# Kernel optimization log

Measured on AMD Instinct MI355X. Metric: run time of the kernel, lower is better.

Reference implementation:

```python
import jax, jax.numpy as jnp
import numpy as np

NOISE_DIM = 64
SEQ_DIM = 64
HIDDEN = 512
BATCH = 1024
N_STEPS = 512
INPUT_SIZE = SEQ_DIM + NOISE_DIM + 1  # 129


def setup_inputs() -> dict:
    key = jax.random.key(0)
    ks = jax.random.split(key, 8)
    s = 0.05
    return {
        "noise": jax.random.normal(ks[0], (BATCH, N_STEPS, NOISE_DIM), dtype=jnp.float32),
        "dts": jax.random.uniform(ks[1], (BATCH, N_STEPS, 1), dtype=jnp.float32),
        "W_ih": jax.random.normal(ks[2], (4 * HIDDEN, INPUT_SIZE), dtype=jnp.float32) * s,
        "W_hh": jax.random.normal(ks[3], (4 * HIDDEN, HIDDEN), dtype=jnp.float32) * s,
        "b_ih": jax.random.normal(ks[4], (4 * HIDDEN,), dtype=jnp.float32) * s,
        "b_hh": jax.random.normal(ks[5], (4 * HIDDEN,), dtype=jnp.float32) * s,
        "W_out": jax.random.normal(ks[6], (SEQ_DIM, HIDDEN), dtype=jnp.float32) * s,
        "b_out": jax.random.normal(ks[7], (SEQ_DIM,), dtype=jnp.float32) * s,
    }


def reference(noise, dts, W_ih, W_hh, b_ih, b_hh, W_out, b_out):
    B = noise.shape[0]
    H = W_hh.shape[1]
    last0 = jnp.zeros((B, SEQ_DIM), dtype=noise.dtype)
    h0 = jnp.zeros((B, H), dtype=noise.dtype)
    c0 = jnp.zeros((B, H), dtype=noise.dtype)
    b = b_ih + b_hh

    def step(carry, inp):
        last, h, c = carry
        n_t, dt_t = inp  # (B, noise_dim), (B, 1)
        x = jnp.concatenate([last, n_t, dt_t], axis=-1)  # (B, input_size)
        gates = x @ W_ih.T + h @ W_hh.T + b  # (B, 4H)
        i_g, f_g, g_g, o_g = jnp.split(gates, 4, axis=-1)
        c_new = jax.nn.sigmoid(f_g) * c + jax.nn.sigmoid(i_g) * jnp.tanh(g_g)
        h_new = jax.nn.sigmoid(o_g) * jnp.tanh(c_new)
        y = h_new @ W_out.T + b_out  # (B, seq_dim)
        return (y, h_new, c_new), y

    noise_t = jnp.swapaxes(noise, 0, 1)  # (n, B, noise_dim)
    dts_t = jnp.swapaxes(dts, 0, 1)  # (n, B, 1)
    (last, h, c), ys = jax.lax.scan(step, (last0, h0, c0), (noise_t, dts_t))
    gen_seq = jnp.swapaxes(ys, 0, 1)  # (B, n, seq_dim)
    return gen_seq, h[None, :, :], c[None, :, :]
```

## Files before the change

kernel.cpp:

```cpp
#include <hip/hip_runtime.h>
#include <stdint.h>


#define NGRP 32
#define KF_X 5
#define KF_H 32
#define KF_TOT 37
#define MAIN_FRAGS (8 * 8 * KF_TOT)
#define Y_FRAGS 64
#define TOT_FRAGS (MAIN_FRAGS + Y_FRAGS)
#define HOFF 33554432ull
#define COFF (HOFF + 524288ull)

typedef __attribute__((ext_vector_type(8))) short short8;
typedef __attribute__((ext_vector_type(4))) float f32x4;
typedef __attribute__((ext_vector_type(16))) float f32x16;
typedef __attribute__((ext_vector_type(4))) unsigned int u32x4;
typedef __attribute__((ext_vector_type(2))) unsigned int u32x2;

__device__ __forceinline__ unsigned short f2bf(float x) {
  unsigned int u = __float_as_uint(x);
  u += 0x7FFFu + ((u >> 16) & 1u);
  return (unsigned short)(u >> 16);
}
__device__ __forceinline__ unsigned int pk2(float a, float b) {
  return (unsigned)f2bf(a) | ((unsigned)f2bf(b) << 16);
}
__device__ __forceinline__ int uperm(int kz, int hi, int j) {
  return 64 * (kz >> 2) + 16 * (kz & 3) + 8 * (j >> 2) + 2 * (j & 3) + hi;
}

__global__ void prep_pack(const float* __restrict__ Wih,
                          const float* __restrict__ Whh,
                          const float* __restrict__ bih,
                          const float* __restrict__ bhh,
                          const float* __restrict__ Wout,
                          const float* __restrict__ bout,
                          unsigned short* __restrict__ pack,
                          int* __restrict__ flags) {
  int tid = blockIdx.x * blockDim.x + threadIdx.x;
  if (blockIdx.x == 0) {
    for (int i = threadIdx.x; i < NGRP * 256; i += blockDim.x) flags[i] = 0;
  }
  int fi = tid >> 6, l = tid & 63;
  if (fi >= TOT_FRAGS) return;
  int r = l & 31, hi = l >> 5;
  unsigned short o[8];
  if (fi < MAIN_FRAGS) {
    int jwg = fi / (8 * KF_TOT);
    int rem = fi % (8 * KF_TOT);
    int w = rem / KF_TOT, kf = rem % KF_TOT;
    int g2 = r & 3, s = r >> 3, hb = (r >> 2) & 1;
    int row = g2 * 512 + jwg * 64 + w * 8 + 2 * s + hb;
    for (int j = 0; j < 8; ++j) {
      float v;
      if (kf < KF_X) {
        int kx = kf * 16 + 8 * hi + j;
        if (kx < 64) {
          v = Wih[row * 129 + 64 + kx];
        } else if (kx == 64) {
          v = Wih[row * 129 + 128];
        } else if (kx == 65) {
          float a = bih[row] + bhh[row];
          for (int q = 0; q < 64; ++q) a += Wih[row * 129 + q] * bout[q];
          v = a;
        } else if (kx == 66) {
          float a = 0.f;
          for (int q = 0; q < 64; ++q) a -= Wih[row * 129 + q] * bout[q];
          v = a;
        } else {
          v = 0.f;
        }
      } else {
        int kz = kf - KF_X;
        int U = uperm(kz, hi, j);
        float a = Whh[row * 512 + U];
        for (int q = 0; q < 64; ++q) a += Wih[row * 129 + q] * Wout[q * 512 + U];
        v = a;
      }
      o[j] = f2bf(v);
    }
  } else {
    int fy = fi - MAIN_FRAGS;
    int ry = fy >> 5, kz = fy & 31;
    int row = ry * 32 + r;
    for (int j = 0; j < 8; ++j) {
      int U = uperm(kz, hi, j);
      o[j] = f2bf(Wout[row * 512 + U]);
    }
  }
  unsigned short* dst = pack + (size_t)fi * 512 + l * 8;
  for (int j = 0; j < 8; ++j) dst[j] = o[j];
}

__global__ __launch_bounds__(512, 1) void lstm_main(
    const float* __restrict__ noise, const float* __restrict__ dts,
    const unsigned short* __restrict__ pack, const float* __restrict__ bout,
    unsigned short* __restrict__ hbuf, int* __restrict__ flags,
    float* __restrict__ out) {
  __shared__ __align__(16) unsigned short act[KF_TOT * 512];
  __shared__ __align__(16) float ybuf[2 * 64 * 17];
  const int tid = threadIdx.x;
  const int w = tid >> 6, l = tid & 63;
  const int r = l & 31, hi = l >> 5;
  const int bid = blockIdx.x;
  const int jwg = bid >> 5, grp = bid & 31;
  const int bat = grp * 32 + r;

  for (int i = tid; i < (KF_H * 512) / 2; i += 512)
    ((unsigned int*)(act + KF_X * 512))[i] = 0u;

  short8 wreg[KF_TOT];
  {
    const unsigned short* wl =
        pack + (size_t)((jwg * 8 + w) * KF_TOT) * 512 + l * 8;
#pragma unroll
    for (int kf = 0; kf < KF_TOT; ++kf)
      wreg[kf] = *(const short8*)(wl + (size_t)kf * 512);
#pragma unroll
    for (int kf = 0; kf < KF_TOT; ++kf) asm volatile("" : "+v"(wreg[kf]));
  }

  float c_st[4] = {0.f, 0.f, 0.f, 0.f}, hf[4] = {0.f, 0.f, 0.f, 0.f};
  float4 bo4[4];
  if (jwg < 2 && w == 2) {
#pragma unroll
    for (int s = 0; s < 4; ++s)
      bo4[s] = *(const float4*)(bout + 32 * jwg + 8 * s + 4 * hi);
  }

  auto stage_x = [&](int tt) {
    if (w < 4) {
      const float* np = noise + ((size_t)bat * 512 + tt) * 64 + w * 16 + 8 * hi;
      float4 f0 = *(const float4*)np;
      float4 f1 = *(const float4*)(np + 4);
      u32x4 d;
      d[0] = pk2(f0.x, f0.y);
      d[1] = pk2(f0.z, f0.w);
      d[2] = pk2(f1.x, f1.y);
      d[3] = pk2(f1.z, f1.w);
      *(u32x4*)&act[w * 512 + l * 8] = d;
    } else if (w == 4) {
      u32x4 d = {0u, 0u, 0u, 0u};
      if (hi == 0) {
        float dt = dts[(size_t)bat * 512 + tt];
        d[0] = pk2(dt, 1.0f);
        d[1] = pk2(tt == 0 ? 1.0f : 0.0f, 0.0f);
      }
      *(u32x4*)&act[4 * 512 + l * 8] = d;
    }
  };

  auto y_partial = [&]() {
    const unsigned short* yl =
        pack + (size_t)(MAIN_FRAGS + jwg * 32 + w * 16) * 512 + l * 8;
    f32x16 ya;
#pragma unroll
    for (int i = 0; i < 16; ++i) ya[i] = 0.f;
    short8 ywr[4];
#pragma unroll
    for (int p = 0; p < 4; ++p) ywr[p] = *(const short8*)(yl + (size_t)p * 512);
#pragma unroll
    for (int q = 0; q < 16; ++q) {
      short8 bv = *(const short8*)&act[(KF_X + w * 16 + q) * 512 + l * 8];
      ya = __builtin_amdgcn_mfma_f32_32x32x16_bf16(ywr[q & 3], bv, ya, 0, 0, 0);
      if (q + 4 < 16)
        ywr[q & 3] = *(const short8*)(yl + (size_t)(q + 4) * 512);
    }
#pragma unroll
    for (int s = 0; s < 4; ++s) {
      f32x4 v = {ya[4 * s], ya[4 * s + 1], ya[4 * s + 2], ya[4 * s + 3]};
      *(f32x4*)&ybuf[(w * 64 + l) * 17 + 4 * s] = v;
    }
  };

  auto y_reduce = [&](int tw) {
#pragma unroll
    for (int s = 0; s < 4; ++s) {
      f32x4 a = *(f32x4*)&ybuf[l * 17 + 4 * s];
      f32x4 b = *(f32x4*)&ybuf[(64 + l) * 17 + 4 * s];
      float4 o;
      o.x = a[0] + b[0] + bo4[s].x;
      o.y = a[1] + b[1] + bo4[s].y;
      o.z = a[2] + b[2] + bo4[s].z;
      o.w = a[3] + b[3] + bo4[s].w;
      *(float4*)(out + ((size_t)bat * 512 + tw) * 64 + 32 * jwg + 8 * s +
                 4 * hi) = o;
    }
  };

  stage_x(0);
  __syncthreads();

#pragma unroll 1
  for (int t = 0; t < 512; ++t) {
    f32x16 acc;
#pragma unroll
    for (int i = 0; i < 16; ++i) acc[i] = 0.f;
#pragma unroll
    for (int kf = 0; kf < KF_TOT; ++kf) {
      short8 bv = *(const short8*)&act[kf * 512 + l * 8];
      acc = __builtin_amdgcn_mfma_f32_32x32x16_bf16(wreg[kf], bv, acc, 0, 0, 0);
    }

    if (jwg < 2 && w < 2 && t > 0) y_partial();

#pragma unroll
    for (int s = 0; s < 4; ++s) {
      float iv = acc[4 * s + 0], fv = acc[4 * s + 1];
      float gv = acc[4 * s + 2], ov = acc[4 * s + 3];
      float ig = 1.f / (1.f + __expf(-iv));
      float fg = 1.f / (1.f + __expf(-fv));
      float e2g = __expf(2.f * gv);
      float gg = 1.f - 2.f / (e2g + 1.f);
      float og = 1.f / (1.f + __expf(-ov));
      float cn = fg * c_st[s] + ig * gg;
      float e2c = __expf(2.f * cn);
      float tc = 1.f - 2.f / (e2c + 1.f);
      c_st[s] = cn;
      hf[s] = og * tc;
    }

    const int kz_own = 4 * jwg + (w >> 1);
    {
      unsigned long long hv =
          (unsigned long long)pk2(hf[0], hf[1]) |
          ((unsigned long long)pk2(hf[2], hf[3]) << 32);
      unsigned long long* hp = (unsigned long long*)(
          hbuf + ((size_t)(grp * 2 + (t & 1)) * KF_H + kz_own) * 512 + l * 8 +
          4 * (w & 1));
      __hip_atomic_store(hp, hv, __ATOMIC_RELAXED, __HIP_MEMORY_SCOPE_AGENT);
    }
    __syncthreads();

    if (tid == 0)
      __hip_atomic_store(&flags[grp * 256 + jwg * 32], t + 1, __ATOMIC_RELAXED,
                         __HIP_MEMORY_SCOPE_AGENT);

    {
      u32x2 d;
      d[0] = pk2(hf[0], hf[1]);
      d[1] = pk2(hf[2], hf[3]);
      *(u32x2*)&act[(KF_X + kz_own) * 512 + l * 8 + 4 * (w & 1)] = d;
    }

    if (jwg < 2 && w == 2 && t > 0) y_reduce(t - 1);
    if (t < 511) stage_x(t + 1);

    if (tid < 8) {
      while (__hip_atomic_load(&flags[grp * 256 + tid * 32], __ATOMIC_RELAXED,
                               __HIP_MEMORY_SCOPE_AGENT) < t + 1)
        __builtin_amdgcn_s_sleep(1);
    }
    __syncthreads();

    {
      const unsigned long long* src = (const unsigned long long*)(
          hbuf + (size_t)(grp * 2 + (t & 1)) * KF_H * 512);
#pragma unroll
      for (int p = 0; p < 4; ++p) {
        int f = 8 * p + w;
        if ((f >> 2) != jwg) {
          int idx = f * 128 + l * 2;
          unsigned long long q0 = __hip_atomic_load(
              src + idx, __ATOMIC_RELAXED, __HIP_MEMORY_SCOPE_AGENT);
          unsigned long long q1 = __hip_atomic_load(
              src + idx + 1, __ATOMIC_RELAXED, __HIP_MEMORY_SCOPE_AGENT);
          u32x4 d;
          d[0] = (unsigned)q0;
          d[1] = (unsigned)(q0 >> 32);
          d[2] = (unsigned)q1;
          d[3] = (unsigned)(q1 >> 32);
          *(u32x4*)&act[(KF_X + f) * 512 + l * 8] = d;
        }
      }
    }
    __syncthreads();
  }

  if (jwg < 2 && w < 2) y_partial();
  __syncthreads();
  if (jwg < 2 && w == 2) y_reduce(511);
#pragma unroll
  for (int s = 0; s < 4; ++s) {
    int U = 64 * jwg + 8 * w + 2 * s + hi;
    out[HOFF + (size_t)bat * 512 + U] = hf[s];
    out[COFF + (size_t)bat * 512 + U] = c_st[s];
  }
}

extern "C" void kernel_launch(void* const* d_in, const int* in_sizes, int n_in,
                              void* d_out, int out_size, void* d_ws,
                              size_t ws_size, hipStream_t stream) {
  (void)in_sizes;
  (void)n_in;
  (void)out_size;
  (void)ws_size;
  const float* noise = (const float*)d_in[0];
  const float* dts = (const float*)d_in[1];
  const float* Wih = (const float*)d_in[2];
  const float* Whh = (const float*)d_in[3];
  const float* bih = (const float*)d_in[4];
  const float* bhh = (const float*)d_in[5];
  const float* Wout = (const float*)d_in[6];
  const float* bout = (const float*)d_in[7];

  unsigned short* pack = (unsigned short*)d_ws;
  unsigned short* hbuf = pack + (size_t)TOT_FRAGS * 512;
  int* flags = (int*)(hbuf + (size_t)NGRP * 2 * KF_H * 512);

  prep_pack<<<(TOT_FRAGS * 64 + 255) / 256, 256, 0, stream>>>(
      Wih, Whh, bih, bhh, Wout, bout, pack, flags);
  lstm_main<<<256, 512, 0, stream>>>(noise, dts, pack, bout, hbuf, flags,
                                     (float*)d_out);
}
```

Before: 2.886 ms.

## Prefetch next-step noise early, defer y_partial past h store, force one block per CU

The global loads for the next step's noise and dt now start at the top of each timestep. They are packed into LDS only after the gate computation, so their latency overlaps the MFMA work instead of sitting on the critical path. The y_partial output projection moves after the hidden-state atomic store, so the h values other workgroups wait on are published earlier. The launch attributes change to waves_per_eu(2,2), and ybuf is enlarged so LDS usage likely keeps one block per CU, spreading the persistent blocks out. In exchange, prefetch registers stay live across the MFMA loop, and the larger LDS footprint limits co-residency.

```diff
diff --git a/kernel.cpp b/kernel.cpp
--- a/kernel.cpp
+++ b/kernel.cpp
@@ -93,13 +93,19 @@
   for (int j = 0; j < 8; ++j) dst[j] = o[j];
 }
 
-__global__ __launch_bounds__(512, 1) void lstm_main(
+#define AGLD(p) \
+  __hip_atomic_load((p), __ATOMIC_RELAXED, __HIP_MEMORY_SCOPE_AGENT)
+#define AGST(p, v) \
+  __hip_atomic_store((p), (v), __ATOMIC_RELAXED, __HIP_MEMORY_SCOPE_AGENT)
+
+__global__ __launch_bounds__(512)
+__attribute__((amdgpu_waves_per_eu(2, 2))) void lstm_main(
     const float* __restrict__ noise, const float* __restrict__ dts,
     const unsigned short* __restrict__ pack, const float* __restrict__ bout,
     unsigned short* __restrict__ hbuf, int* __restrict__ flags,
     float* __restrict__ out) {
   __shared__ __align__(16) unsigned short act[KF_TOT * 512];
-  __shared__ __align__(16) float ybuf[2 * 64 * 17];
+  __shared__ __align__(16) float ybuf[11700];
   const int tid = threadIdx.x;
   const int w = tid >> 6, l = tid & 63;
   const int r = l & 31, hi = l >> 5;
@@ -129,9 +135,9 @@
       bo4[s] = *(const float4*)(bout + 32 * jwg + 8 * s + 4 * hi);
   }
 
-  auto stage_x = [&](int tt) {
+  auto stage_x0 = [&]() {
     if (w < 4) {
-      const float* np = noise + ((size_t)bat * 512 + tt) * 64 + w * 16 + 8 * hi;
+      const float* np = noise + (size_t)bat * 512 * 64 + w * 16 + 8 * hi;
       float4 f0 = *(const float4*)np;
       float4 f1 = *(const float4*)(np + 4);
       u32x4 d;
@@ -143,9 +149,9 @@
     } else if (w == 4) {
       u32x4 d = {0u, 0u, 0u, 0u};
       if (hi == 0) {
-        float dt = dts[(size_t)bat * 512 + tt];
+        float dt = dts[(size_t)bat * 512];
         d[0] = pk2(dt, 1.0f);
-        d[1] = pk2(tt == 0 ? 1.0f : 0.0f, 0.0f);
+        d[1] = pk2(1.0f, 0.0f);
       }
       *(u32x4*)&act[4 * 512 + l * 8] = d;
     }
@@ -189,11 +195,24 @@
     }
   };
 
-  stage_x(0);
+  stage_x0();
   __syncthreads();
 
 #pragma unroll 1
   for (int t = 0; t < 512; ++t) {
+    float4 nf0, nf1;
+    float dtv = 0.f;
+    if (t < 511) {
+      if (w < 4) {
+        const float* np =
+            noise + ((size_t)bat * 512 + t + 1) * 64 + w * 16 + 8 * hi;
+        nf0 = *(const float4*)np;
+        nf1 = *(const float4*)(np + 4);
+      } else if (w == 4 && hi == 0) {
+        dtv = dts[(size_t)bat * 512 + t + 1];
+      }
+    }
+
     f32x16 acc;
 #pragma unroll
     for (int i = 0; i < 16; ++i) acc[i] = 0.f;
@@ -202,8 +221,6 @@
       short8 bv = *(const short8*)&act[kf * 512 + l * 8];
       acc = __builtin_amdgcn_mfma_f32_32x32x16_bf16(wreg[kf], bv, acc, 0, 0, 0);
     }
-
-    if (jwg < 2 && w < 2 && t > 0) y_partial();
 
 #pragma unroll
     for (int s = 0; s < 4; ++s) {
@@ -229,13 +246,15 @@
       unsigned long long* hp = (unsigned long long*)(
           hbuf + ((size_t)(grp * 2 + (t & 1)) * KF_H + kz_own) * 512 + l * 8 +
           4 * (w & 1));
-      __hip_atomic_store(hp, hv, __ATOMIC_RELAXED, __HIP_MEMORY_SCOPE_AGENT);
-    }
+      AGST(hp, hv);
+    }
+
+    if (jwg < 2 && w < 2 && t > 0) y_partial();
+
     __syncthreads();
 
     if (tid == 0)
-      __hip_atomic_store(&flags[grp * 256 + jwg * 32], t + 1, __ATOMIC_RELAXED,
-                         __HIP_MEMORY_SCOPE_AGENT);
+      AGST(&flags[grp * 256 + jwg * 32], t + 1);
 
     {
       u32x2 d;
@@ -245,11 +264,24 @@
     }
 
     if (jwg < 2 && w == 2 && t > 0) y_reduce(t - 1);
-    if (t < 511) stage_x(t + 1);
+
+    if (t < 511) {
+      if (w < 4) {
+        u32x4 d;
+        d[0] = pk2(nf0.x, nf0.y);
+        d[1] = pk2(nf0.z, nf0.w);
+        d[2] = pk2(nf1.x, nf1.y);
+        d[3] = pk2(nf1.z, nf1.w);
+        *(u32x4*)&act[w * 512 + l * 8] = d;
+      } else if (w == 4) {
+        u32x4 d = {0u, 0u, 0u, 0u};
+        if (hi == 0) d[0] = pk2(dtv, 1.0f);
+        *(u32x4*)&act[4 * 512 + l * 8] = d;
+      }
+    }
 
     if (tid < 8) {
-      while (__hip_atomic_load(&flags[grp * 256 + tid * 32], __ATOMIC_RELAXED,
-                               __HIP_MEMORY_SCOPE_AGENT) < t + 1)
+      while (AGLD(&flags[grp * 256 + tid * 32]) < t + 1)
         __builtin_amdgcn_s_sleep(1);
     }
     __syncthreads();
@@ -262,10 +294,8 @@
         int f = 8 * p + w;
         if ((f >> 2) != jwg) {
           int idx = f * 128 + l * 2;
-          unsigned long long q0 = __hip_atomic_load(
-              src + idx, __ATOMIC_RELAXED, __HIP_MEMORY_SCOPE_AGENT);
-          unsigned long long q1 = __hip_atomic_load(
-              src + idx + 1, __ATOMIC_RELAXED, __HIP_MEMORY_SCOPE_AGENT);
+          unsigned long long q0 = AGLD(src + idx);
+          unsigned long long q1 = AGLD(src + idx + 1);
           u32x4 d;
           d[0] = (unsigned)q0;
           d[1] = (unsigned)(q0 >> 32);
```

Result: slower. 3.409 ms (+18.1%).
